# Kernel tuning notes

Hardware: AMD Instinct MI355X
Metric: run time of the kernel (lower is better)

Reference implementation:

```python
import jax, jax.numpy as jnp
import numpy as np

NUM_EMBEDDINGS = 1024
EMBEDDING_DIM = 64
COMMITMENT_COST = 0.25


def setup_inputs() -> dict:
    key = jax.random.key(0)
    k1, k2 = jax.random.split(key)
    inputs = jax.random.normal(k1, (32, 4096, EMBEDDING_DIM), dtype=jnp.float32)
    embeddings = jax.random.normal(k2, (NUM_EMBEDDINGS, EMBEDDING_DIM), dtype=jnp.float32)
    return {"inputs": inputs, "embeddings": embeddings}


def _l2_normalize(x, axis=-1, eps=1e-12):
    # matches F.normalize(p=2): x / max(||x||, eps)
    n = jnp.sqrt(jnp.sum(x * x, axis=axis, keepdims=True))
    return x / jnp.maximum(n, eps)


def reference(inputs, embeddings):
    input_shape = inputs.shape
    flat = inputs.reshape(-1, EMBEDDING_DIM)            # [N, D]
    flat_n = _l2_normalize(flat, axis=1)                # [N, D]
    emb_n = _l2_normalize(embeddings, axis=1)           # [K, D]

    # squared euclidean distances between normalized vectors: [N, K]
    d = (jnp.sum(flat_n * flat_n, axis=1, keepdims=True)
         + jnp.sum(emb_n * emb_n, axis=1)
         - 2.0 * flat_n @ emb_n.T)
    idx = jnp.argmin(d, axis=1)                         # [N] int

    quantized = embeddings[idx]                         # [N, D] gather

    e_latent_loss = jnp.mean((jax.lax.stop_gradient(quantized) - flat) ** 2)
    # straight-through estimator
    quantized_ste = flat + jax.lax.stop_gradient(quantized - flat)
    q_latent_loss = jnp.mean((quantized_ste - jax.lax.stop_gradient(flat)) ** 2)
    vq_loss = q_latent_loss + COMMITMENT_COST * e_latent_loss

    quantized_out = quantized_ste.reshape(input_shape)

    counts = jnp.bincount(idx, length=NUM_EMBEDDINGS).astype(jnp.float32)
    avg_probs = counts / idx.shape[0]
    perplexity = jnp.exp(-jnp.sum(avg_probs * jnp.log(avg_probs + 1e-10)))
    codebook_usage = jnp.sum(avg_probs > 0).astype(jnp.float32) / NUM_EMBEDDINGS

    return quantized_out, idx, vq_loss, perplexity, codebook_usage
```

## Files before the change

kernel.cpp:

```cpp
#include <hip/hip_runtime.h>
#include <hip/hip_bf16.h>

#define NQ       131072
#define KC       1024
#define DIM      64
#define MARGIN_A 7.5e-5f
#define RGRID    2048

typedef __attribute__((ext_vector_type(8))) short  s8bf;
typedef __attribute__((ext_vector_type(4))) float  f32x4;

union BF8 { s8bf v; unsigned short u[8]; };

__device__ __forceinline__ unsigned short f2bf_u(float f) {
    union { __hip_bfloat16 h; unsigned short u; } cv;
    cv.h = __float2bfloat16(f);
    return cv.u;
}
__device__ __forceinline__ float bfu2f(unsigned short u) {
    union { __hip_bfloat16 h; unsigned short u; } cv;
    cv.u = u;
    return __bfloat162float(cv.h);
}

__global__ __launch_bounds__(256) void k_prep(const float* __restrict__ emb,
                                              unsigned short* __restrict__ wB,
                                              double* __restrict__ eT,
                                              double* __restrict__ wB2D,
                                              int* __restrict__ counts,
                                              int* __restrict__ nflag,
                                              float* __restrict__ lossp) {
    const int tid = threadIdx.x;
    if (blockIdx.x == 0) {
        #pragma unroll
        for (int i = 0; i < 4; ++i) counts[tid * 4 + i] = 0;
        if (tid == 0) { *nflag = 0; *lossp = 0.f; }
    }
    int c = blockIdx.x * 256 + tid;
    if (c >= KC) return;
    float e[DIM];
    const float4* ep = reinterpret_cast<const float4*>(emb + (size_t)c * DIM);
    #pragma unroll
    for (int i = 0; i < 16; ++i) {
        float4 t = ep[i];
        e[4*i+0] = t.x; e[4*i+1] = t.y; e[4*i+2] = t.z; e[4*i+3] = t.w;
    }
    float s = 0.f;
    #pragma unroll
    for (int i = 0; i < DIM; ++i) s += e[i] * e[i];
    float inv = 1.0f / fmaxf(sqrtf(s), 1e-12f);
    const int t = c >> 4, col = c & 15;
    #pragma unroll
    for (int k = 0; k < DIM; ++k) {
        float h = e[k] * inv;
        unsigned short hi = f2bf_u(h);
        unsigned short lo = f2bf_u(h - bfu2f(hi));
        int s_ = k >> 5, g = (k >> 3) & 3, j = k & 7;
        int ln = col + 16 * g;
        wB[((t*4 + s_*2 + 0) * 64 + ln) * 8 + j] = hi;
        wB[((t*4 + s_*2 + 1) * 64 + ln) * 8 + j] = lo;
    }
    double sd = 0.0;
    #pragma unroll
    for (int i = 0; i < DIM; ++i) sd += (double)e[i] * (double)e[i];
    double dnd = fmax(sqrt(sd), 1e-12);
    double b2 = 0.0;
    #pragma unroll
    for (int i = 0; i < DIM; ++i) {
        double eh = (double)e[i] / dnd;
        eT[(size_t)i * KC + c] = eh;
        b2 += eh * eh;
    }
    wB2D[c] = b2;
}

__global__ __launch_bounds__(256) void k_assign(const float* __restrict__ inp,
                                                const unsigned short* __restrict__ wB,
                                                float* __restrict__ idx_out,
                                                int* __restrict__ flag_list,
                                                int* __restrict__ nflag) {
    const int tid  = threadIdx.x;
    const int lane = tid & 63, wv = tid >> 6;
    const int col  = lane & 15, g  = lane >> 4;
    const int qbase = blockIdx.x * 256 + wv * 64;

    BF8 ah[4][2], al[4][2];
    #pragma unroll
    for (int s = 0; s < 4; ++s) {
        const float4* q4 = reinterpret_cast<const float4*>(inp + (size_t)(qbase + 16*s + col) * DIM);
        float4 xa = q4[2*g], xb = q4[2*g + 1], ya = q4[8 + 2*g], yb = q4[9 + 2*g];
        float x[16] = { xa.x, xa.y, xa.z, xa.w, xb.x, xb.y, xb.z, xb.w,
                        ya.x, ya.y, ya.z, ya.w, yb.x, yb.y, yb.z, yb.w };
        float sq = 0.f;
        #pragma unroll
        for (int i = 0; i < 16; ++i) sq += x[i] * x[i];
        sq += __shfl_xor(sq, 16);
        sq += __shfl_xor(sq, 32);
        float ninv = -1.0f / fmaxf(sqrtf(sq), 1e-12f);
        #pragma unroll
        for (int i = 0; i < 8; ++i) {
            float h0 = x[i] * ninv, h1 = x[8 + i] * ninv;
            unsigned short hi0 = f2bf_u(h0);
            unsigned short hi1 = f2bf_u(h1);
            ah[s][0].u[i] = hi0;  al[s][0].u[i] = f2bf_u(h0 - bfu2f(hi0));
            ah[s][1].u[i] = hi1;  al[s][1].u[i] = f2bf_u(h1 - bfu2f(hi1));
        }
    }

    int best[4][4], best2[4][4];
    #pragma unroll
    for (int s = 0; s < 4; ++s)
        #pragma unroll
        for (int r = 0; r < 4; ++r) { best[s][r] = 0x7FFFFFFF; best2[s][r] = 0x7FFFFFFF; }

    const s8bf* wBs = reinterpret_cast<const s8bf*>(wB);
    s8bf nb0 = wBs[0*64 + lane];
    s8bf nb1 = wBs[1*64 + lane];
    s8bf nb2 = wBs[2*64 + lane];
    s8bf nb3 = wBs[3*64 + lane];

    for (int gt = 0; gt < 64; ++gt) {
        s8bf bh0 = nb0, bl0 = nb1, bh1 = nb2, bl1 = nb3;
        if (gt < 63) {
            const s8bf* p = wBs + (gt + 1) * 4 * 64 + lane;
            nb0 = p[0]; nb1 = p[64]; nb2 = p[128]; nb3 = p[192];
        }
        #pragma unroll
        for (int s = 0; s < 4; ++s) {
            f32x4 acc = {1.5f, 1.5f, 1.5f, 1.5f};
            acc = __builtin_amdgcn_mfma_f32_16x16x32_bf16(ah[s][0].v, bh0, acc, 0, 0, 0);
            acc = __builtin_amdgcn_mfma_f32_16x16x32_bf16(ah[s][1].v, bh1, acc, 0, 0, 0);
            acc = __builtin_amdgcn_mfma_f32_16x16x32_bf16(ah[s][0].v, bl0, acc, 0, 0, 0);
            acc = __builtin_amdgcn_mfma_f32_16x16x32_bf16(ah[s][1].v, bl1, acc, 0, 0, 0);
            acc = __builtin_amdgcn_mfma_f32_16x16x32_bf16(al[s][0].v, bh0, acc, 0, 0, 0);
            acc = __builtin_amdgcn_mfma_f32_16x16x32_bf16(al[s][1].v, bh1, acc, 0, 0, 0);
            #pragma unroll
            for (int r = 0; r < 4; ++r) {
                int p = (__float_as_int(acc[r]) & 0xFFFFFFC0) | gt;
                int bo = best[s][r];
                int b2n;
                asm("v_med3_i32 %0, %1, %2, %3"
                    : "=v"(b2n) : "v"(bo), "v"(best2[s][r]), "v"(p));
                best2[s][r] = b2n;
                best[s][r]  = min(bo, p);
            }
        }
    }

    int colb[4][4];
    #pragma unroll
    for (int s = 0; s < 4; ++s)
        #pragma unroll
        for (int r = 0; r < 4; ++r) colb[s][r] = col;

    #pragma unroll
    for (int s = 0; s < 4; ++s) {
        #pragma unroll
        for (int off = 1; off < 16; off <<= 1) {
            #pragma unroll
            for (int r = 0; r < 4; ++r) {
                int ob  = __shfl_xor(best[s][r],  off);
                int ob2 = __shfl_xor(best2[s][r], off);
                int oc  = __shfl_xor(colb[s][r],  off);
                int bo  = best[s][r];
                colb[s][r]  = (ob < bo) ? oc : colb[s][r];
                best[s][r]  = min(bo, ob);
                best2[s][r] = min(min(best2[s][r], ob2), max(bo, ob));
            }
        }
        #pragma unroll
        for (int r = 0; r < 4; ++r) {
            if (col == r) {
                int   q  = qbase + 16*s + 4*g + r;
                int   pk = best[s][r];
                float a1 = __int_as_float(pk & 0xFFFFFFC0);
                float a2 = __int_as_float(best2[s][r] & 0xFFFFFFC0);
                int code = ((pk & 63) << 4) | colb[s][r];
                idx_out[q] = (float)code;
                if (a2 - a1 < MARGIN_A) {
                    int slot = atomicAdd(nflag, 1);
                    flag_list[slot] = q;
                }
            }
        }
    }
}

__global__ __launch_bounds__(256) void k_rescue(const float* __restrict__ inp,
                                                const double* __restrict__ eT,
                                                const double* __restrict__ wB2D,
                                                const int* __restrict__ flag_list,
                                                const int* __restrict__ nflag,
                                                float* __restrict__ idx_out) {
    __shared__ double xh[DIM];
    __shared__ double Ash;
    __shared__ double sdw[4];
    __shared__ int    siw[4];
    const int tid = threadIdx.x;
    const int lane = tid & 63, wv = tid >> 6;
    const int n = *nflag;

    for (int j = blockIdx.x; j < n; j += gridDim.x) {
        const int q = flag_list[j];
        if (tid < 64) {
            double xv = (double)inp[(size_t)q * DIM + tid];
            double s = xv * xv;
            #pragma unroll
            for (int off = 32; off; off >>= 1) s += __shfl_xor(s, off);
            double dn = fmax(sqrt(s), 1e-12);
            double h  = xv / dn;
            xh[tid] = h;
            double a = h * h;
            #pragma unroll
            for (int off = 32; off; off >>= 1) a += __shfl_xor(a, off);
            if (tid == 0) Ash = a;
        }
        __syncthreads();
        const double A = Ash;

        double dot0 = 0.0, dot1 = 0.0, dot2 = 0.0, dot3 = 0.0;
        #pragma unroll 8
        for (int i = 0; i < DIM; ++i) {
            double xi = xh[i];
            const double* row = eT + (size_t)i * KC + tid;
            dot0 += xi * row[0];
            dot1 += xi * row[256];
            dot2 += xi * row[512];
            dot3 += xi * row[768];
        }
        double bd = 1e300; int bi = 1 << 30;
        double d0 = (A + wB2D[tid      ]) - 2.0 * dot0;
        double d1 = (A + wB2D[tid + 256]) - 2.0 * dot1;
        double d2 = (A + wB2D[tid + 512]) - 2.0 * dot2;
        double d3 = (A + wB2D[tid + 768]) - 2.0 * dot3;
        if (d0 < bd) { bd = d0; bi = tid;       }
        if (d1 < bd) { bd = d1; bi = tid + 256; }
        if (d2 < bd) { bd = d2; bi = tid + 512; }
        if (d3 < bd) { bd = d3; bi = tid + 768; }
        #pragma unroll
        for (int off = 1; off < 64; off <<= 1) {
            double od = __shfl_xor(bd, off);
            int    oi = __shfl_xor(bi, off);
            if (od < bd || (od == bd && oi < bi)) { bd = od; bi = oi; }
        }
        if (lane == 0) { sdw[wv] = bd; siw[wv] = bi; }
        __syncthreads();
        if (tid == 0) {
            double B = sdw[0]; int I = siw[0];
            #pragma unroll
            for (int i = 1; i < 4; ++i)
                if (sdw[i] < B || (sdw[i] == B && siw[i] < I)) { B = sdw[i]; I = siw[i]; }
            idx_out[q] = (float)I;
        }
        __syncthreads();
    }
}

__global__ __launch_bounds__(256) void k_gather_loss(const float* __restrict__ inp,
                                                     const float* __restrict__ emb,
                                                     const float* __restrict__ idx_out,
                                                     float* __restrict__ qout,
                                                     float* __restrict__ loss,
                                                     int* __restrict__ counts) {
    __shared__ int h[KC];
    const int tid = threadIdx.x;
    for (int i = tid; i < KC; i += 256) h[i] = 0;
    __syncthreads();

    const int gid = blockIdx.x * 256 + tid;
    float lsum = 0.f;
    for (int e4 = gid; e4 < NQ * 16; e4 += 524288) {
        int   qi = e4 >> 4;
        int   d4 = e4 & 15;
        int   k  = ((int)idx_out[qi]) & (KC - 1);
        float4 qv = reinterpret_cast<const float4*>(emb + (size_t)k * DIM)[d4];
        float4 fv = reinterpret_cast<const float4*>(inp)[e4];
        float ux = qv.x - fv.x, uy = qv.y - fv.y, uz = qv.z - fv.z, uw = qv.w - fv.w;
        lsum += ux*ux + uy*uy + uz*uz + uw*uw;
        reinterpret_cast<float4*>(qout)[e4] = qv;
        if (d4 == 0) atomicAdd(&h[k], 1);
    }
    __syncthreads();
    for (int i = tid; i < KC; i += 256) {
        int v = h[i];
        if (v) atomicAdd(&counts[i], v);
    }
    #pragma unroll
    for (int off = 32; off; off >>= 1) lsum += __shfl_xor(lsum, off);
    __shared__ float wsum[4];
    int wid = tid >> 6, lane = tid & 63;
    if (lane == 0) wsum[wid] = lsum;
    __syncthreads();
    if (tid == 0)
        atomicAdd(loss, (wsum[0] + wsum[1]) + (wsum[2] + wsum[3]));
}

__global__ __launch_bounds__(1024) void k_stats2(const int* __restrict__ counts,
                                                 float* __restrict__ out3) {
    int t = threadIdx.x;
    int c = counts[t];
    float p    = (float)c * (1.0f / (float)NQ);
    float ent  = p * logf(p + 1e-10f);
    float used = (c > 0) ? 1.0f : 0.0f;
    #pragma unroll
    for (int off = 32; off; off >>= 1) {
        ent  += __shfl_xor(ent, off);
        used += __shfl_xor(used, off);
    }
    __shared__ float se[16], su[16];
    int w = t >> 6, l = t & 63;
    if (l == 0) { se[w] = ent; su[w] = used; }
    __syncthreads();
    if (t == 0) {
        float E = 0.f, U = 0.f;
        #pragma unroll
        for (int i = 0; i < 16; ++i) { E += se[i]; U += su[i]; }
        float L = out3[0];
        out3[0] = L * 1.25f / 8388608.0f;
        out3[1] = expf(-E);
        out3[2] = U * (1.0f / 1024.0f);
    }
}

extern "C" void kernel_launch(void* const* d_in, const int* in_sizes, int n_in,
                              void* d_out, int out_size, void* d_ws, size_t ws_size,
                              hipStream_t stream) {
    const float* inp = (const float*)d_in[0];
    const float* emb = (const float*)d_in[1];

    float*  qout      = (float*)d_out;
    int*    flag_list = (int*)d_out;
    double* eT        = (double*)((float*)d_out + 1048576);
    float*  idx_out   = (float*)d_out + 8388608;
    float*  out3      = (float*)d_out + 8519680;

    int*            counts = (int*)d_ws;
    unsigned short* wB     = (unsigned short*)((char*)d_ws + 4096);
    double*         wB2D   = (double*)((char*)d_ws + 266240);
    int*            nflag  = (int*)((char*)d_ws + 274432);

    hipLaunchKernelGGL(k_prep,        dim3(4),     dim3(256),  0, stream,
                       emb, wB, eT, wB2D, counts, nflag, out3);
    hipLaunchKernelGGL(k_assign,      dim3(512),   dim3(256),  0, stream,
                       inp, wB, idx_out, flag_list, nflag);
    hipLaunchKernelGGL(k_rescue,      dim3(RGRID), dim3(256),  0, stream,
                       inp, eT, wB2D, flag_list, nflag, idx_out);
    hipLaunchKernelGGL(k_gather_loss, dim3(2048),  dim3(256),  0, stream,
                       inp, emb, idx_out, qout, out3, counts);
    hipLaunchKernelGGL(k_stats2,      dim3(1),     dim3(1024), 0, stream, counts, out3);
}
```

Baseline: 118.3 us.

## Parallelize codebook prep, double-buffer assign loads, fuse stats into gather via last-block

Measured after the change: 150.0 us. 1.27x slower.

```diff
diff --git a/kernel.cpp b/kernel.cpp
--- a/kernel.cpp
+++ b/kernel.cpp
@@ -6,6 +6,7 @@
 #define DIM      64
 #define MARGIN_A 7.5e-5f
 #define RGRID    2048
+#define GGRID    2048
 
 typedef __attribute__((ext_vector_type(8))) short  s8bf;
 typedef __attribute__((ext_vector_type(4))) float  f32x4;
@@ -23,55 +24,44 @@
     return __bfloat162float(cv.h);
 }
 
-__global__ __launch_bounds__(256) void k_prep(const float* __restrict__ emb,
-                                              unsigned short* __restrict__ wB,
-                                              double* __restrict__ eT,
-                                              double* __restrict__ wB2D,
-                                              int* __restrict__ counts,
-                                              int* __restrict__ nflag,
-                                              float* __restrict__ lossp) {
-    const int tid = threadIdx.x;
-    if (blockIdx.x == 0) {
-        #pragma unroll
-        for (int i = 0; i < 4; ++i) counts[tid * 4 + i] = 0;
-        if (tid == 0) { *nflag = 0; *lossp = 0.f; }
-    }
-    int c = blockIdx.x * 256 + tid;
-    if (c >= KC) return;
-    float e[DIM];
-    const float4* ep = reinterpret_cast<const float4*>(emb + (size_t)c * DIM);
-    #pragma unroll
-    for (int i = 0; i < 16; ++i) {
-        float4 t = ep[i];
-        e[4*i+0] = t.x; e[4*i+1] = t.y; e[4*i+2] = t.z; e[4*i+3] = t.w;
-    }
-    float s = 0.f;
-    #pragma unroll
-    for (int i = 0; i < DIM; ++i) s += e[i] * e[i];
-    float inv = 1.0f / fmaxf(sqrtf(s), 1e-12f);
+__global__ __launch_bounds__(64) void k_prep(const float* __restrict__ emb,
+                                             unsigned short* __restrict__ wB,
+                                             double* __restrict__ eT,
+                                             double* __restrict__ wB2D,
+                                             int* __restrict__ counts,
+                                             int* __restrict__ nflag,
+                                             float* __restrict__ lossp,
+                                             int* __restrict__ done) {
+    const int c = blockIdx.x;
+    const int i = threadIdx.x;
+    if (i == 0) counts[c] = 0;
+    if (c == 0 && i == 0) { *nflag = 0; *lossp = 0.f; *done = 0; }
+
+    float e = emb[(size_t)c * DIM + i];
+    float sq = e * e;
+    #pragma unroll
+    for (int off = 1; off < 64; off <<= 1) sq += __shfl_xor(sq, off);
+    float inv = 1.0f / fmaxf(sqrtf(sq), 1e-12f);
+    float h = e * inv;
+    unsigned short hi = f2bf_u(h);
+    unsigned short lo = f2bf_u(h - bfu2f(hi));
     const int t = c >> 4, col = c & 15;
-    #pragma unroll
-    for (int k = 0; k < DIM; ++k) {
-        float h = e[k] * inv;
-        unsigned short hi = f2bf_u(h);
-        unsigned short lo = f2bf_u(h - bfu2f(hi));
-        int s_ = k >> 5, g = (k >> 3) & 3, j = k & 7;
-        int ln = col + 16 * g;
-        wB[((t*4 + s_*2 + 0) * 64 + ln) * 8 + j] = hi;
-        wB[((t*4 + s_*2 + 1) * 64 + ln) * 8 + j] = lo;
-    }
-    double sd = 0.0;
-    #pragma unroll
-    for (int i = 0; i < DIM; ++i) sd += (double)e[i] * (double)e[i];
+    const int s_ = i >> 5, g = (i >> 3) & 3, j = i & 7;
+    const int ln = col + 16 * g;
+    wB[((t*4 + s_*2 + 0) * 64 + ln) * 8 + j] = hi;
+    wB[((t*4 + s_*2 + 1) * 64 + ln) * 8 + j] = lo;
+
+    double ed = (double)e;
+    double sd = ed * ed;
+    #pragma unroll
+    for (int off = 1; off < 64; off <<= 1) sd += __shfl_xor(sd, off);
     double dnd = fmax(sqrt(sd), 1e-12);
-    double b2 = 0.0;
-    #pragma unroll
-    for (int i = 0; i < DIM; ++i) {
-        double eh = (double)e[i] / dnd;
-        eT[(size_t)i * KC + c] = eh;
-        b2 += eh * eh;
-    }
-    wB2D[c] = b2;
+    double eh  = ed / dnd;
+    eT[(size_t)i * KC + c] = eh;
+    double b2 = eh * eh;
+    #pragma unroll
+    for (int off = 1; off < 64; off <<= 1) b2 += __shfl_xor(b2, off);
+    if (i == 0) wB2D[c] = b2;
 }
 
 __global__ __launch_bounds__(256) void k_assign(const float* __restrict__ inp,
@@ -114,38 +104,47 @@
         for (int r = 0; r < 4; ++r) { best[s][r] = 0x7FFFFFFF; best2[s][r] = 0x7FFFFFFF; }
 
     const s8bf* wBs = reinterpret_cast<const s8bf*>(wB);
-    s8bf nb0 = wBs[0*64 + lane];
-    s8bf nb1 = wBs[1*64 + lane];
-    s8bf nb2 = wBs[2*64 + lane];
-    s8bf nb3 = wBs[3*64 + lane];
-
-    for (int gt = 0; gt < 64; ++gt) {
-        s8bf bh0 = nb0, bl0 = nb1, bh1 = nb2, bl1 = nb3;
-        if (gt < 63) {
-            const s8bf* p = wBs + (gt + 1) * 4 * 64 + lane;
-            nb0 = p[0]; nb1 = p[64]; nb2 = p[128]; nb3 = p[192];
-        }
-        #pragma unroll
-        for (int s = 0; s < 4; ++s) {
-            f32x4 acc = {1.5f, 1.5f, 1.5f, 1.5f};
-            acc = __builtin_amdgcn_mfma_f32_16x16x32_bf16(ah[s][0].v, bh0, acc, 0, 0, 0);
-            acc = __builtin_amdgcn_mfma_f32_16x16x32_bf16(ah[s][1].v, bh1, acc, 0, 0, 0);
-            acc = __builtin_amdgcn_mfma_f32_16x16x32_bf16(ah[s][0].v, bl0, acc, 0, 0, 0);
-            acc = __builtin_amdgcn_mfma_f32_16x16x32_bf16(ah[s][1].v, bl1, acc, 0, 0, 0);
-            acc = __builtin_amdgcn_mfma_f32_16x16x32_bf16(al[s][0].v, bh0, acc, 0, 0, 0);
-            acc = __builtin_amdgcn_mfma_f32_16x16x32_bf16(al[s][1].v, bh1, acc, 0, 0, 0);
-            #pragma unroll
-            for (int r = 0; r < 4; ++r) {
-                int p = (__float_as_int(acc[r]) & 0xFFFFFFC0) | gt;
-                int bo = best[s][r];
-                int b2n;
-                asm("v_med3_i32 %0, %1, %2, %3"
-                    : "=v"(b2n) : "v"(bo), "v"(best2[s][r]), "v"(p));
-                best2[s][r] = b2n;
-                best[s][r]  = min(bo, p);
-            }
-        }
-    }
+
+    s8bf A0 = wBs[0*64 + lane], A1 = wBs[1*64 + lane];
+    s8bf A2 = wBs[2*64 + lane], A3 = wBs[3*64 + lane];
+    s8bf B0 = wBs[4*64 + lane], B1 = wBs[5*64 + lane];
+    s8bf B2 = wBs[6*64 + lane], B3 = wBs[7*64 + lane];
+
+    #define ARGMIN_TILE(BH0, BL0, BH1, BL1, GT)                                        \
+        _Pragma("unroll")                                                              \
+        for (int s = 0; s < 4; ++s) {                                                  \
+            f32x4 acc = {1.5f, 1.5f, 1.5f, 1.5f};                                      \
+            acc = __builtin_amdgcn_mfma_f32_16x16x32_bf16(ah[s][0].v, BH0, acc, 0,0,0);\
+            acc = __builtin_amdgcn_mfma_f32_16x16x32_bf16(ah[s][1].v, BH1, acc, 0,0,0);\
+            acc = __builtin_amdgcn_mfma_f32_16x16x32_bf16(ah[s][0].v, BL0, acc, 0,0,0);\
+            acc = __builtin_amdgcn_mfma_f32_16x16x32_bf16(ah[s][1].v, BL1, acc, 0,0,0);\
+            acc = __builtin_amdgcn_mfma_f32_16x16x32_bf16(al[s][0].v, BH0, acc, 0,0,0);\
+            acc = __builtin_amdgcn_mfma_f32_16x16x32_bf16(al[s][1].v, BH1, acc, 0,0,0);\
+            _Pragma("unroll")                                                          \
+            for (int r = 0; r < 4; ++r) {                                              \
+                int p = (__float_as_int(acc[r]) & 0xFFFFFFC0) | (GT);                  \
+                int bo = best[s][r];                                                   \
+                int b2n;                                                               \
+                asm("v_med3_i32 %0, %1, %2, %3"                                        \
+                    : "=v"(b2n) : "v"(bo), "v"(best2[s][r]), "v"(p));                  \
+                best2[s][r] = b2n;                                                     \
+                best[s][r]  = min(bo, p);                                              \
+            }                                                                          \
+        }
+
+    for (int gt = 0; gt < 64; gt += 2) {
+        ARGMIN_TILE(A0, A1, A2, A3, gt)
+        if (gt + 2 < 64) {
+            const s8bf* p = wBs + (size_t)(gt + 2) * 4 * 64 + lane;
+            A0 = p[0]; A1 = p[64]; A2 = p[128]; A3 = p[192];
+        }
+        ARGMIN_TILE(B0, B1, B2, B3, gt + 1)
+        if (gt + 3 < 64) {
+            const s8bf* p = wBs + (size_t)(gt + 3) * 4 * 64 + lane;
+            B0 = p[0]; B1 = p[64]; B2 = p[128]; B3 = p[192];
+        }
+    }
+    #undef ARGMIN_TILE
 
     int colb[4][4];
     #pragma unroll
@@ -260,9 +259,11 @@
                                                      const float* __restrict__ emb,
                                                      const float* __restrict__ idx_out,
                                                      float* __restrict__ qout,
-                                                     float* __restrict__ loss,
-                                                     int* __restrict__ counts) {
+                                                     float* __restrict__ out3,
+                                                     int* __restrict__ counts,
+                                                     int* __restrict__ done) {
     __shared__ int h[KC];
+    __shared__ int lastf;
     const int tid = threadIdx.x;
     for (int i = tid; i < KC; i += 256) h[i] = 0;
     __syncthreads();
@@ -291,31 +292,34 @@
     int wid = tid >> 6, lane = tid & 63;
     if (lane == 0) wsum[wid] = lsum;
     __syncthreads();
-    if (tid == 0)
-        atomicAdd(loss, (wsum[0] + wsum[1]) + (wsum[2] + wsum[3]));
-}
-
-__global__ __launch_bounds__(1024) void k_stats2(const int* __restrict__ counts,
-                                                 float* __restrict__ out3) {
-    int t = threadIdx.x;
-    int c = counts[t];
-    float p    = (float)c * (1.0f / (float)NQ);
-    float ent  = p * logf(p + 1e-10f);
-    float used = (c > 0) ? 1.0f : 0.0f;
+    if (tid == 0) {
+        atomicAdd(out3, (wsum[0] + wsum[1]) + (wsum[2] + wsum[3]));
+        __threadfence();
+        int d = atomicAdd(done, 1);
+        lastf = (d == GGRID - 1);
+    }
+    __syncthreads();
+    if (!lastf) return;
+
+    float ent = 0.f, used = 0.f;
+    for (int i = tid; i < KC; i += 256) {
+        int cc = atomicAdd(&counts[i], 0);
+        float p = (float)cc * (1.0f / (float)NQ);
+        ent  += p * logf(p + 1e-10f);
+        used += (cc > 0) ? 1.0f : 0.0f;
+    }
     #pragma unroll
     for (int off = 32; off; off >>= 1) {
         ent  += __shfl_xor(ent, off);
         used += __shfl_xor(used, off);
     }
-    __shared__ float se[16], su[16];
-    int w = t >> 6, l = t & 63;
-    if (l == 0) { se[w] = ent; su[w] = used; }
-    __syncthreads();
-    if (t == 0) {
-        float E = 0.f, U = 0.f;
-        #pragma unroll
-        for (int i = 0; i < 16; ++i) { E += se[i]; U += su[i]; }
-        float L = out3[0];
+    __shared__ float se[4], su[4];
+    if (lane == 0) { se[wid] = ent; su[wid] = used; }
+    __syncthreads();
+    if (tid == 0) {
+        float E = (se[0] + se[1]) + (se[2] + se[3]);
+        float U = (su[0] + su[1]) + (su[2] + su[3]);
+        float L = atomicAdd(out3, 0.0f);
         out3[0] = L * 1.25f / 8388608.0f;
         out3[1] = expf(-E);
         out3[2] = U * (1.0f / 1024.0f);
@@ -338,14 +342,14 @@
     unsigned short* wB     = (unsigned short*)((char*)d_ws + 4096);
     double*         wB2D   = (double*)((char*)d_ws + 266240);
     int*            nflag  = (int*)((char*)d_ws + 274432);
-
-    hipLaunchKernelGGL(k_prep,        dim3(4),     dim3(256),  0, stream,
-                       emb, wB, eT, wB2D, counts, nflag, out3);
-    hipLaunchKernelGGL(k_assign,      dim3(512),   dim3(256),  0, stream,
+    int*            done   = (int*)((char*)d_ws + 274436);
+
+    hipLaunchKernelGGL(k_prep,        dim3(1024),  dim3(64),  0, stream,
+                       emb, wB, eT, wB2D, counts, nflag, out3, done);
+    hipLaunchKernelGGL(k_assign,      dim3(512),   dim3(256), 0, stream,
                        inp, wB, idx_out, flag_list, nflag);
-    hipLaunchKernelGGL(k_rescue,      dim3(RGRID), dim3(256),  0, stream,
+    hipLaunchKernelGGL(k_rescue,      dim3(RGRID), dim3(256), 0, stream,
                        inp, eT, wB2D, flag_list, nflag, idx_out);
-    hipLaunchKernelGGL(k_gather_loss, dim3(2048),  dim3(256),  0, stream,
-                       inp, emb, idx_out, qout, out3, counts);
-    hipLaunchKernelGGL(k_stats2,      dim3(1),     dim3(1024), 0, stream, counts, out3);
-}
+    hipLaunchKernelGGL(k_gather_loss, dim3(GGRID), dim3(256), 0, stream,
+                       inp, emb, idx_out, qout, out3, counts, done);
+}
```
